# Kernel tuning notes

Measured on AMD Instinct MI355X. Metric: run time of the kernel, lower is better.

Reference implementation:

```python
import jax, jax.numpy as jnp
import numpy as np

NUM_STEPS = 151
DIRECT_PRED_WEIGHT = 1.0
CLASS_NUM_PER_BATCH = 64
BATCH_SUPPORT_NUM_PER_CLASS = 8
SUPPORT = CLASS_NUM_PER_BATCH * BATCH_SUPPORT_NUM_PER_CLASS  # 512
BATCH = 65536
TARGET = BATCH - SUPPORT  # 65024
NUM_CLASSES = 64


def setup_inputs() -> dict:
    key = jax.random.key(0)
    k1, k2, k3 = jax.random.split(key, 3)
    direct_cls_logits = jax.random.normal(k1, (TARGET, NUM_CLASSES), dtype=jnp.float32)
    # similarities in [0,1) subset of the [-1,1] histogram support
    inner_product = jax.random.uniform(k2, (TARGET, SUPPORT), dtype=jnp.float32)
    cls_labels = jax.random.randint(k3, (BATCH,), 0, NUM_CLASSES, dtype=jnp.int64)
    return {"direct_cls_logits": direct_cls_logits,
            "inner_product": inner_product,
            "cls_labels": cls_labels}


def reference(direct_cls_logits, inner_product, cls_labels):
    step = 2.0 / (NUM_STEPS - 1)          # histogram bin width
    tsize = NUM_STEPS                      # t = -1, -1+step, ..., 1
    half = (NUM_STEPS - 1) // 2            # index offset so t_k = -1 + k*step

    support_labels = cls_labels[:SUPPORT]
    target_labels = cls_labels[SUPPORT:]

    # direct classification loss (mean cross entropy)
    logp = jax.nn.log_softmax(direct_cls_logits, axis=-1)
    nll = -jnp.take_along_axis(logp, target_labels[:, None], axis=1)[:, 0]
    direct_loss = jnp.mean(nll) * DIRECT_PRED_WEIGHT

    # pairwise positive/negative masks, flattened over all pairs
    mask_pos = (support_labels[None, :] == target_labels[:, None]).reshape(-1)
    m_pos = mask_pos.astype(jnp.float32)
    m_neg = 1.0 - m_pos
    pos_num = m_pos.sum()
    neg_num = m_neg.sum()

    # soft histogram via linear-interpolation scatter-add.
    # Original: bin k (t_k = floor(s/step)*step) gets (s - t_k)/step,
    #           bin k+1 gets (t_{k+1} - s)/step; bin tsize is dropped.
    s = inner_product.reshape(-1)
    kf = jnp.floor(s / step)
    frac = s / step - kf                   # (s - t_k)/step in [0,1)
    k = (kf).astype(jnp.int32) + half      # bin index of floor node

    def soft_hist(m, size):
        h = jnp.zeros((tsize + 1,), dtype=jnp.float32)
        h = h.at[k].add(frac * m)
        h = h.at[k + 1].add((1.0 - frac) * m)
        return h[:tsize] / size

    hist_pos = soft_hist(m_pos, pos_num)
    hist_neg = soft_hist(m_neg, neg_num)

    # CDF of positive histogram (triangular-matrix trick == cumsum)
    hist_pos_cdf = jnp.cumsum(hist_pos)
    histo_loss = jnp.sum(hist_neg * hist_pos_cdf)

    return histo_loss, direct_loss
```

## Files before the change

### kernel.cpp

```cpp
#include <hip/hip_runtime.h>

#define SUPPORT 512
#define TARGET  65024
#define NCLS    64
#define NQUAD   (TARGET / 4)
#define GS_ROWS 64
#define GS_BLK  (TARGET / GS_ROWS)
#define PH_BLK  2032
#define DR_BLK  1024

struct Accum {
    float hist_fr_sp[8][80];
    float hist_cnt_sp[8][80];
    float sum_all[8];
    float nll_sum[8];
    float spos;
    float pos_num;
    int   cls_off[NCLS + 1];
    int   cls_col[SUPPORT];
};
#define ZERO_WORDS (8 * 80 * 2 + 8 + 8)

__device__ __forceinline__ void lds_fadd(float* p, float v) {
    __hip_atomic_fetch_add(p, v, __ATOMIC_RELAXED, __HIP_MEMORY_SCOPE_WORKGROUP);
}

__global__ void prep_kernel(const int* __restrict__ labels, Accum* ws) {
    __shared__ int sh_cnt[NCLS], sh_off[NCLS], cur[NCLS];
    const int t = threadIdx.x;
    int* wsi = (int*)ws;
    for (int i = t; i < ZERO_WORDS; i += 512) wsi[i] = 0;
    if (t < NCLS) { sh_cnt[t] = 0; cur[t] = 0; }
    __syncthreads();
    const int c = labels[t];
    atomicAdd(&sh_cnt[c], 1);
    __syncthreads();
    if (t == 0) {
        int o = 0;
        for (int i = 0; i < NCLS; ++i) { sh_off[i] = o; ws->cls_off[i] = o; o += sh_cnt[i]; }
        ws->cls_off[NCLS] = o;
    }
    __syncthreads();
    const int slot = atomicAdd(&cur[c], 1);
    ws->cls_col[sh_off[c] + slot] = t;
}

__global__ __launch_bounds__(256) void phdir_kernel(const float* __restrict__ ip,
                                                    const float* __restrict__ logits,
                                                    const int* __restrict__ labels,
                                                    Accum* __restrict__ ws) {
    const int tid = threadIdx.x;
    if (blockIdx.x < PH_BLK) {
        __shared__ float hfr[76][8];
        __shared__ float hcnt[76][8];
        __shared__ int   colL[SUPPORT];
        __shared__ int   offL[NCLS + 1];
        for (int i = tid; i < 76 * 8; i += 256) {
            (&hfr[0][0])[i] = 0.0f;
            (&hcnt[0][0])[i] = 0.0f;
        }
        for (int i = tid; i < SUPPORT; i += 256) colL[i] = ws->cls_col[i];
        if (tid <= NCLS) offL[tid] = ws->cls_off[tid];
        __syncthreads();

        const int row = (blockIdx.x * 256 + tid) >> 3;
        const int sl  = tid & 7;
        {
            const int c    = labels[SUPPORT + row];
            const int base = offL[c];
            const int cnt  = offL[c + 1] - base;
            const float* rptr = ip + (size_t)row * SUPPORT;
            for (int j = sl; j < cnt; j += 8) {
                const float s  = rptr[colL[base + j]];
                const float u  = s * 75.0f;
                const float fl = floorf(u);
                const int idx  = (int)fl;
                lds_fadd(&hfr[idx][sl],  u - fl);
                lds_fadd(&hcnt[idx][sl], 1.0f);
            }
        }
        __syncthreads();
        if (tid < 76) {
            float a = 0.0f, b = 0.0f;
            #pragma unroll
            for (int r = 0; r < 8; ++r) { a += hfr[tid][r]; b += hcnt[tid][r]; }
            if (a != 0.0f) unsafeAtomicAdd(&ws->hist_fr_sp[blockIdx.x & 7][tid], a);
            if (b != 0.0f) unsafeAtomicAdd(&ws->hist_cnt_sp[blockIdx.x & 7][tid], b);
        }
    } else {
        __shared__ float red[4];
        const int bid  = blockIdx.x - PH_BLK;
        const int wid  = tid >> 6;
        const int lane = tid & 63;
        const int sub  = lane >> 4;
        const int grpb = lane & ~15;

        float lsum = 0.0f;
        for (int q = bid * 4 + wid; q < NQUAD; q += DR_BLK * 4) {
            const float4 x = reinterpret_cast<const float4*>(logits)[q * 64 + lane];
            const int lab  = labels[SUPPORT + q * 4 + sub];
            float m = fmaxf(fmaxf(x.x, x.y), fmaxf(x.z, x.w));
            #pragma unroll
            for (int off = 1; off < 16; off <<= 1) m = fmaxf(m, __shfl_xor(m, off));
            float e = __expf(x.x - m) + __expf(x.y - m) + __expf(x.z - m) + __expf(x.w - m);
            #pragma unroll
            for (int off = 1; off < 16; off <<= 1) e += __shfl_xor(e, off);
            const int l3 = lab & 3;
            const float sel = l3 == 0 ? x.x : l3 == 1 ? x.y : l3 == 2 ? x.z : x.w;
            const float xl = __shfl(sel, grpb + (lab >> 2));
            if ((lane & 15) == 0) lsum += m + __logf(e) - xl;
        }
        #pragma unroll
        for (int off = 1; off < 64; off <<= 1) lsum += __shfl_xor(lsum, off);
        if (lane == 0) red[wid] = lsum;
        __syncthreads();
        if (tid == 0)
            unsafeAtomicAdd(&ws->nll_sum[bid & 7], red[0] + red[1] + red[2] + red[3]);
    }
}

__global__ __launch_bounds__(256, 4) void stream_kernel(const float* __restrict__ ip,
                                                        Accum* __restrict__ ws) {
    __shared__ float2 tab[76 * 16];
    __shared__ float Sfr[80], Cnt[80];
    __shared__ float Atab[80], Btab[80];
    __shared__ float red[4];
    const int tid = threadIdx.x;

    if (tid < 76) {
        float a = 0.0f, b = 0.0f;
        #pragma unroll
        for (int r = 0; r < 8; ++r) { a += ws->hist_fr_sp[r][tid]; b += ws->hist_cnt_sp[r][tid]; }
        Sfr[tid] = a; Cnt[tid] = b;
    }
    if (tid >= 76 && tid < 80) { Sfr[tid] = 0.0f; Cnt[tid] = 0.0f; }
    __syncthreads();
    if (tid == 0) {
        float prevS = 0.0f, prevN = 0.0f, cacc = 0.0f;
        double sp = 0.0, pn = 0.0;
        for (int i = 0; i <= 76; ++i) {
            const float Si = (i < 76) ? Sfr[i] : 0.0f;
            const float Ni = (i < 76) ? Cnt[i] : 0.0f;
            const float Hi = Si + prevN - prevS;
            cacc += Hi;
            if (i >= 1) {
                const int k = i - 1;
                Atab[k] = cacc + (float)k * Hi;
                Btab[k] = Hi;
                sp += (double)prevN * cacc - (double)prevS * Hi;
            }
            pn += (double)Ni;
            prevS = Si; prevN = Ni;
        }
        if (blockIdx.x == 0) { ws->spos = (float)sp; ws->pos_num = (float)pn; }
    }
    __syncthreads();
    const int c16 = tid & 15;
    for (int i = tid; i < 76 * 16; i += 256)
        tab[i] = make_float2(Atab[i >> 4], Btab[i >> 4]);
    __syncthreads();

    const float4* base = reinterpret_cast<const float4*>(ip)
                       + (size_t)blockIdx.x * (GS_ROWS * 128) + tid;

    float sa0 = 0.0f, sb0 = 0.0f, sa1 = 0.0f, sb1 = 0.0f;
    float4 qa0, qa1, qa2, qa3, qa4, qa5, qa6, qa7;
    float4 qb0, qb1, qb2, qb3, qb4, qb5, qb6, qb7;

#define LDA(T) { qa0 = base[((T)+0)*256]; qa1 = base[((T)+1)*256]; \
                 qa2 = base[((T)+2)*256]; qa3 = base[((T)+3)*256]; \
                 qa4 = base[((T)+4)*256]; qa5 = base[((T)+5)*256]; \
                 qa6 = base[((T)+6)*256]; qa7 = base[((T)+7)*256]; }
#define LDB(T) { qb0 = base[((T)+0)*256]; qb1 = base[((T)+1)*256]; \
                 qb2 = base[((T)+2)*256]; qb3 = base[((T)+3)*256]; \
                 qb4 = base[((T)+4)*256]; qb5 = base[((T)+5)*256]; \
                 qb6 = base[((T)+6)*256]; qb7 = base[((T)+7)*256]; }
#define PE(S, SA, SB) { const float u = (S) * 75.0f; const int idx = (int)u;   \
                        const float2 ab = tab[(idx << 4) + c16];               \
                        SA += ab.x; SB = fmaf(u, ab.y, SB); }
#define P1(Q) { PE(Q.x, sa0, sb0) PE(Q.y, sa1, sb1) PE(Q.z, sa0, sb0) PE(Q.w, sa1, sb1) }
#define PA()  { P1(qa0) P1(qa1) P1(qa2) P1(qa3) P1(qa4) P1(qa5) P1(qa6) P1(qa7) }
#define PB()  { P1(qb0) P1(qb1) P1(qb2) P1(qb3) P1(qb4) P1(qb5) P1(qb6) P1(qb7) }

    LDA(0);
    LDB(8);
    PA();  LDA(16);
    PB();  LDB(24);
    PA();
    PB();

#undef LDA
#undef LDB
#undef PE
#undef P1
#undef PA
#undef PB

    float s_all = (sa0 + sa1) - (sb0 + sb1);
    #pragma unroll
    for (int off = 1; off < 64; off <<= 1) s_all += __shfl_xor(s_all, off);
    if ((tid & 63) == 0) red[tid >> 6] = s_all;
    __syncthreads();
    if (tid == 0)
        unsafeAtomicAdd(&ws->sum_all[blockIdx.x & 7], red[0] + red[1] + red[2] + red[3]);
}

__global__ void final_kernel(const Accum* __restrict__ ws, float* __restrict__ out) {
    if (threadIdx.x == 0 && blockIdx.x == 0) {
        double S = 0.0, nll = 0.0;
        for (int i = 0; i < 8; ++i) {
            S   += (double)ws->sum_all[i];
            nll += (double)ws->nll_sum[i];
        }
        const double pos = (double)ws->pos_num;
        const double tot = (double)TARGET * (double)SUPPORT;
        out[0] = (float)((S - (double)ws->spos) / (pos * (tot - pos)));
        out[1] = (float)(nll / (double)TARGET);
    }
}

extern "C" void kernel_launch(void* const* d_in, const int* in_sizes, int n_in,
                              void* d_out, int out_size, void* d_ws, size_t ws_size,
                              hipStream_t stream) {
    const float* logits = (const float*)d_in[0];
    const float* ip     = (const float*)d_in[1];
    const int*   labels = (const int*)d_in[2];
    float* out = (float*)d_out;
    Accum* ws  = (Accum*)d_ws;

    prep_kernel<<<1, 512, 0, stream>>>(labels, ws);
    phdir_kernel<<<PH_BLK + DR_BLK, 256, 0, stream>>>(ip, logits, labels, ws);
    stream_kernel<<<GS_BLK, 256, 0, stream>>>(ip, ws);
    final_kernel<<<1, 64, 0, stream>>>(ws, out);
}
```

Measured before the change: 73.87 us.

## Drop prep kernel, build class index per block, deepen stream prefetch

Removes the single-block prep kernel and instead has every phdir histogram block count labels and build the class-sorted column list in shared memory; workspace zeroing moves to hipMemsetAsync. This drops one kernel launch from the serial chain, at the cost of redundant per-block label reads and shared atomics. Separately, the stream kernel now issues three batches of 8 float4 loads up front instead of two, raising the number of memory requests in flight at the cost of more registers.

```diff
diff --git a/kernel.cpp b/kernel.cpp
--- a/kernel.cpp
+++ b/kernel.cpp
@@ -16,33 +16,10 @@
     float nll_sum[8];
     float spos;
     float pos_num;
-    int   cls_off[NCLS + 1];
-    int   cls_col[SUPPORT];
 };
-#define ZERO_WORDS (8 * 80 * 2 + 8 + 8)
 
 __device__ __forceinline__ void lds_fadd(float* p, float v) {
     __hip_atomic_fetch_add(p, v, __ATOMIC_RELAXED, __HIP_MEMORY_SCOPE_WORKGROUP);
-}
-
-__global__ void prep_kernel(const int* __restrict__ labels, Accum* ws) {
-    __shared__ int sh_cnt[NCLS], sh_off[NCLS], cur[NCLS];
-    const int t = threadIdx.x;
-    int* wsi = (int*)ws;
-    for (int i = t; i < ZERO_WORDS; i += 512) wsi[i] = 0;
-    if (t < NCLS) { sh_cnt[t] = 0; cur[t] = 0; }
-    __syncthreads();
-    const int c = labels[t];
-    atomicAdd(&sh_cnt[c], 1);
-    __syncthreads();
-    if (t == 0) {
-        int o = 0;
-        for (int i = 0; i < NCLS; ++i) { sh_off[i] = o; ws->cls_off[i] = o; o += sh_cnt[i]; }
-        ws->cls_off[NCLS] = o;
-    }
-    __syncthreads();
-    const int slot = atomicAdd(&cur[c], 1);
-    ws->cls_col[sh_off[c] + slot] = t;
 }
 
 __global__ __launch_bounds__(256) void phdir_kernel(const float* __restrict__ ip,
@@ -55,12 +32,30 @@
         __shared__ float hcnt[76][8];
         __shared__ int   colL[SUPPORT];
         __shared__ int   offL[NCLS + 1];
+        __shared__ int   cntL[NCLS], curL[NCLS];
         for (int i = tid; i < 76 * 8; i += 256) {
             (&hfr[0][0])[i] = 0.0f;
             (&hcnt[0][0])[i] = 0.0f;
         }
-        for (int i = tid; i < SUPPORT; i += 256) colL[i] = ws->cls_col[i];
-        if (tid <= NCLS) offL[tid] = ws->cls_off[tid];
+        if (tid < NCLS) cntL[tid] = 0;
+        __syncthreads();
+        {
+            const int j0 = tid, j1 = tid + 256;
+            atomicAdd(&cntL[labels[j0]], 1);
+            atomicAdd(&cntL[labels[j1]], 1);
+        }
+        __syncthreads();
+        if (tid == 0) {
+            int o = 0;
+            for (int i = 0; i < NCLS; ++i) { offL[i] = o; curL[i] = o; o += cntL[i]; }
+            offL[NCLS] = o;
+        }
+        __syncthreads();
+        {
+            const int j0 = tid, j1 = tid + 256;
+            colL[atomicAdd(&curL[labels[j0]], 1)] = j0;
+            colL[atomicAdd(&curL[labels[j1]], 1)] = j1;
+        }
         __syncthreads();
 
         const int row = (blockIdx.x * 256 + tid) >> 3;
@@ -166,6 +161,7 @@
     float sa0 = 0.0f, sb0 = 0.0f, sa1 = 0.0f, sb1 = 0.0f;
     float4 qa0, qa1, qa2, qa3, qa4, qa5, qa6, qa7;
     float4 qb0, qb1, qb2, qb3, qb4, qb5, qb6, qb7;
+    float4 qc0, qc1, qc2, qc3, qc4, qc5, qc6, qc7;
 
 #define LDA(T) { qa0 = base[((T)+0)*256]; qa1 = base[((T)+1)*256]; \
                  qa2 = base[((T)+2)*256]; qa3 = base[((T)+3)*256]; \
@@ -175,26 +171,34 @@
                  qb2 = base[((T)+2)*256]; qb3 = base[((T)+3)*256]; \
                  qb4 = base[((T)+4)*256]; qb5 = base[((T)+5)*256]; \
                  qb6 = base[((T)+6)*256]; qb7 = base[((T)+7)*256]; }
+#define LDC(T) { qc0 = base[((T)+0)*256]; qc1 = base[((T)+1)*256]; \
+                 qc2 = base[((T)+2)*256]; qc3 = base[((T)+3)*256]; \
+                 qc4 = base[((T)+4)*256]; qc5 = base[((T)+5)*256]; \
+                 qc6 = base[((T)+6)*256]; qc7 = base[((T)+7)*256]; }
 #define PE(S, SA, SB) { const float u = (S) * 75.0f; const int idx = (int)u;   \
                         const float2 ab = tab[(idx << 4) + c16];               \
                         SA += ab.x; SB = fmaf(u, ab.y, SB); }
 #define P1(Q) { PE(Q.x, sa0, sb0) PE(Q.y, sa1, sb1) PE(Q.z, sa0, sb0) PE(Q.w, sa1, sb1) }
 #define PA()  { P1(qa0) P1(qa1) P1(qa2) P1(qa3) P1(qa4) P1(qa5) P1(qa6) P1(qa7) }
 #define PB()  { P1(qb0) P1(qb1) P1(qb2) P1(qb3) P1(qb4) P1(qb5) P1(qb6) P1(qb7) }
+#define PC()  { P1(qc0) P1(qc1) P1(qc2) P1(qc3) P1(qc4) P1(qc5) P1(qc6) P1(qc7) }
 
     LDA(0);
     LDB(8);
-    PA();  LDA(16);
-    PB();  LDB(24);
+    LDC(16);
+    PA();  LDA(24);
+    PB();
+    PC();
     PA();
-    PB();
 
 #undef LDA
 #undef LDB
+#undef LDC
 #undef PE
 #undef P1
 #undef PA
 #undef PB
+#undef PC
 
     float s_all = (sa0 + sa1) - (sb0 + sb1);
     #pragma unroll
@@ -228,7 +232,7 @@
     float* out = (float*)d_out;
     Accum* ws  = (Accum*)d_ws;
 
-    prep_kernel<<<1, 512, 0, stream>>>(labels, ws);
+    hipMemsetAsync(ws, 0, sizeof(Accum), stream);
     phdir_kernel<<<PH_BLK + DR_BLK, 256, 0, stream>>>(ip, logits, labels, ws);
     stream_kernel<<<GS_BLK, 256, 0, stream>>>(ip, ws);
     final_kernel<<<1, 64, 0, stream>>>(ws, out);
```

After: 74.82 us. Within noise of the previous version (+1.3%).
